# Optimization experiments

Measured on AMD Instinct MI355X. Metric: run time of the kernel, lower is better.

The kernel has to match this reference:

```python
import jax, jax.numpy as jnp
import numpy as np

H = 16  # number of heads (init kwarg h)

def vdp_matmul(a, va, b, vb):
    # VDP propagation through a matmul of two independent Gaussian tensors:
    # mean = a @ b ; var = va @ vb + va @ b^2 + a^2 @ vb
    mu = jnp.matmul(a, b)
    var = jnp.matmul(va, vb) + jnp.matmul(va, b * b) + jnp.matmul(a * a, vb)
    return mu, var

def softmax_vdp(a, va):
    # diagonal-Jacobian VDP softmax: p = softmax(a); var = (p(1-p))^2 * va
    p = jax.nn.softmax(a, axis=-1)
    return p, (p * (1.0 - p)) ** 2 * va

def setup_inputs() -> dict:
    key = jax.random.key(0)
    ks = jax.random.split(key, 8)
    B, S, D = 2, 1024, 1024
    sc = 1.0 / np.sqrt(D)
    return {
        "x": jax.random.normal(ks[0], (B, S, D), jnp.float32),
        "var_x": jax.random.uniform(ks[1], (B, S, D), jnp.float32) * 0.1,
        "wq_mu": jax.random.normal(ks[2], (D, D), jnp.float32) * sc,
        "wq_var": jax.random.uniform(ks[3], (D, D), jnp.float32) * 0.01,
        "wk_mu": jax.random.normal(ks[4], (D, D), jnp.float32) * sc,
        "wk_var": jax.random.uniform(ks[5], (D, D), jnp.float32) * 0.01,
        "wv_mu": jax.random.normal(ks[6], (D, D), jnp.float32) * sc,
        "wv_var": jax.random.uniform(ks[7], (D, D), jnp.float32) * 0.01,
    }

def _split_heads(t, h):
    B, S, D = t.shape
    return t.reshape(B, S, h, D // h).transpose(0, 2, 1, 3)  # [B,h,S,dh]

def reference(x, var_x, wq_mu, wq_var, wk_mu, wk_var, wv_mu, wv_var):
    D = x.shape[-1]
    rd = jnp.sqrt(jnp.asarray(D, x.dtype))
    # LinearVDP (bias=False): treat weight^T as the second VDP matmul operand
    q, vq = vdp_matmul(x, var_x, wq_mu.T, wq_var.T)
    k, vk = vdp_matmul(x, var_x, wk_mu.T, wk_var.T)
    v, vv = vdp_matmul(x, var_x, wv_mu.T, wv_var.T)
    q, vq = _split_heads(q, H), _split_heads(vq, H)
    k, vk = _split_heads(k, H), _split_heads(vk, H)
    v, vv = _split_heads(v, H), _split_heads(vv, H)
    # scores: q @ k^T with VDP variance, scaled (masking=False path)
    a, va = vdp_matmul(q, vq, k.transpose(0, 1, 3, 2), vk.transpose(0, 1, 3, 2))
    a, va = a / rd, va / (rd * rd)
    a, va = softmax_vdp(a, va)
    # attention-weighted values with VDP variance
    a, va = vdp_matmul(a, va, v, vv)
    a = a.transpose(0, 2, 1, 3).reshape(x.shape)      # [B,S,D]
    va = va.transpose(0, 2, 1, 3).reshape(x.shape)    # [B,S,D]
    return x + a, va
```

## Files before the change

kernel.cpp:

```cpp
#include <hip/hip_runtime.h>
#include <stdint.h>

typedef unsigned short u16;
typedef __attribute__((ext_vector_type(4))) float f32x4;
typedef __attribute__((ext_vector_type(8))) short s16x8;
typedef __attribute__((ext_vector_type(2))) unsigned u32x2;

#define MFMA16(a,b,c) __builtin_amdgcn_mfma_f32_16x16x32_bf16(a,b,c,0,0,0)

__device__ inline u16 f2b(float f){
  unsigned u = __float_as_uint(f);
  unsigned r = u + 0x7fffu + ((u>>16)&1u);
  return (u16)(r>>16);
}
__device__ inline float b2f(u16 b){
  return __uint_as_float(((unsigned)b)<<16);
}
__device__ inline unsigned cvtpk(float lo, float hi){
  unsigned r;
  asm("v_cvt_pk_bf16_f32 %0, %1, %2" : "=v"(r) : "v"(lo), "v"(hi));
  return r;
}
__device__ inline void load_lds16(const void* g, void* l){
  __builtin_amdgcn_global_load_lds((const __attribute__((address_space(1))) void*)g,
                                   (__attribute__((address_space(3))) void*)l, 16, 0, 0);
}

__global__ void prep_in_kernel(const float* __restrict__ x, const float* __restrict__ vx,
                               const float* __restrict__ w0mu, const float* __restrict__ w0va,
                               const float* __restrict__ w1mu, const float* __restrict__ w1va,
                               const float* __restrict__ w2mu, const float* __restrict__ w2va,
                               u16* __restrict__ xb, u16* __restrict__ acat,
                               u16* __restrict__ wmub, u16* __restrict__ bcat){
  int bid = blockIdx.x;
  if (bid < 2048){
    int i4 = bid*256 + threadIdx.x;
    int base = i4*4;
    int j = base & 1023;
    float4 xv = *(const float4*)(x + base);
    float4 vv = *(const float4*)(vx + base);
    u32x2 xpk = {cvtpk(xv.x,xv.y), cvtpk(xv.z,xv.w)};
    *(u32x2*)(xb + base) = xpk;
    size_t ar = (size_t)(base >> 10)*2048;
    *(u32x2*)(acat + ar + j) = (u32x2){cvtpk(vv.x,vv.y), cvtpk(vv.z,vv.w)};
    *(u32x2*)(acat + ar + 1024 + j) =
        (u32x2){cvtpk(xv.x*xv.x, xv.y*xv.y), cvtpk(xv.z*xv.z, xv.w*xv.w)};
  } else {
    int t = bid - 2048;
    int z = t >> 10;
    int i4 = (t & 1023)*256 + threadIdx.x;
    int base = i4*4;
    const float* wmu = z==0?w0mu:(z==1?w1mu:w2mu);
    const float* wva = z==0?w0va:(z==1?w1va:w2va);
    u16* wb = wmub + (size_t)z*1048576;
    u16* bc = bcat + (size_t)z*2097152;
    int j = base & 1023;
    float4 mu = *(const float4*)(wmu + base);
    float4 va = *(const float4*)(wva + base);
    *(u32x2*)(wb + base) = (u32x2){cvtpk(mu.x,mu.y), cvtpk(mu.z,mu.w)};
    size_t br = (size_t)(base >> 10)*2048;
    *(u32x2*)(bc + br + j) =
        (u32x2){cvtpk(va.x+mu.x*mu.x, va.y+mu.y*mu.y),
                cvtpk(va.z+mu.z*mu.z, va.w+mu.w*mu.w)};
    *(u32x2*)(bc + br + 1024 + j) = (u32x2){cvtpk(va.x,va.y), cvtpk(va.z,va.w)};
  }
}

__global__ __launch_bounds__(256) void gemm_nt6_kernel(
    const u16* __restrict__ xb, const u16* __restrict__ acat,
    const u16* __restrict__ wmub, const u16* __restrict__ bcat,
    u16* __restrict__ cbase){
  int bid = blockIdx.x;
  int z = bid % 6;
  int xy = bid / 6;
  int bx = xy & 15, by = xy >> 4;
  const u16* A = z<3 ? xb : acat;
  int K = z<3 ? 1024 : 2048;
  const u16* B = z<3 ? wmub + (size_t)z*1048576 : bcat + (size_t)(z-3)*2097152;
  u16* C = cbase + (size_t)z*2097152;
  const int N = 1024;
  __shared__ __align__(16) u16 As0[128*32], As1[128*32], As2[128*32];
  __shared__ __align__(16) u16 Bs0[128*32], Bs1[128*32], Bs2[128*32];
  int tid = threadIdx.x;
  int wid = tid>>6, lane = tid&63;
  int wr = wid>>1, wc = wid&1;
  int fr = lane&15, kg = lane>>4;
  int m0 = bx*128, n0 = by*128;
  int srow = lane>>2;
  int scol = (lane&3)*8;

  auto stage = [&](u16* Ad, u16* Bd, int k0){
    #pragma unroll
    for (int c=0;c<2;c++){
      int r = c*64 + wid*16 + srow;
      load_lds16(A + (size_t)(m0+r)*K + k0 + scol, (char*)Ad + (size_t)(c*64+wid*16)*64);
      load_lds16(B + (size_t)(n0+r)*K + k0 + scol, (char*)Bd + (size_t)(c*64+wid*16)*64);
    }
  };

  int nt = K >> 5;
  u16 *Ar=As0, *An=As1, *At=As2, *Br=Bs0, *Bn=Bs1, *Bt=Bs2;
  stage(Ar, Br, 0);
  stage(An, Bn, 32);
  f32x4 acc[4][4] = {};
  for (int t=0; t<nt; t++){
    if (t < nt-1) asm volatile("s_waitcnt vmcnt(4)" ::: "memory");
    else          asm volatile("s_waitcnt vmcnt(0)" ::: "memory");
    __builtin_amdgcn_s_barrier();
    if (t+2 < nt) stage(At, Bt, (t+2)*32);
    s16x8 af[4], bfv[4];
    #pragma unroll
    for (int i=0;i<4;i++){
      af[i]  = *(const s16x8*)(Ar + (wr*64 + i*16 + fr)*32 + kg*8);
      bfv[i] = *(const s16x8*)(Br + (wc*64 + i*16 + fr)*32 + kg*8);
    }
    #pragma unroll
    for (int i=0;i<4;i++)
      #pragma unroll
      for (int j=0;j<4;j++)
        acc[i][j] = MFMA16(bfv[j], af[i], acc[i][j]);
    u16* ta = Ar; Ar = An; An = At; At = ta;
    u16* tb = Br; Br = Bn; Bn = Bt; Bt = tb;
  }
  #pragma unroll
  for (int i=0;i<4;i++){
    int mrow = m0 + wr*64 + i*16 + fr;
    #pragma unroll
    for (int j=0;j<4;j++){
      int ncol = n0 + wc*64 + j*16 + kg*4;
      u32x2 pk = {cvtpk(acc[i][j][0],acc[i][j][1]), cvtpk(acc[i][j][2],acc[i][j][3])};
      *(u32x2*)(C + (size_t)mrow*N + ncol) = pk;
    }
  }
}

__global__ void mid_kernel(const u16* __restrict__ kb, const u16* __restrict__ vkb,
                           u16* __restrict__ kw2,
                           const u16* __restrict__ vb, const u16* __restrict__ vvb,
                           u16* __restrict__ vT, u16* __restrict__ vw2T,
                           u16* __restrict__ vvT){
  __shared__ u16 t[32][33];
  int bid = blockIdx.x;
  if (bid < 6144){
    int z = bid / 2048, wI = bid % 2048;
    int bx = wI & 31, by = wI >> 5;
    u16* out = z==0?vT:(z==1?vw2T:vvT);
    int tx = threadIdx.x & 31, ty = threadIdx.x >> 5;
    int c0 = bx*32, r0 = by*32;
    #pragma unroll
    for (int rr=0; rr<32; rr+=8){
      size_t idx = (size_t)(r0+ty+rr)*1024 + c0+tx;
      u16 val;
      if (z==0)      val = vb[idx];
      else if (z==2) val = vvb[idx];
      else {
        float v  = b2f(vb[idx]);
        float vv = b2f(vvb[idx]);
        val = f2b(vv + v*v);
      }
      t[ty+rr][tx] = val;
    }
    __syncthreads();
    #pragma unroll
    for (int rr=0; rr<32; rr+=8)
      out[(size_t)(c0+ty+rr)*2048 + r0+tx] = t[tx][ty+rr];
  } else {
    int i = (bid - 6144)*256 + threadIdx.x;
    float kk = b2f(kb[i]);
    float vk = b2f(vkb[i]);
    kw2[i] = f2b(vk + kk*kk);
  }
}

__global__ __launch_bounds__(256) void attn_vdp_kernel(
  const u16* __restrict__ qb, const u16* __restrict__ vqb,
  const u16* __restrict__ kb, const u16* __restrict__ kw2, const u16* __restrict__ vkb,
  const u16* __restrict__ vT, const u16* __restrict__ vw2T, const u16* __restrict__ vvT,
  const float* __restrict__ x, float* __restrict__ out0, float* __restrict__ out1){
  int qblk = blockIdx.x, h = blockIdx.y, b = blockIdx.z;
  int wid = threadIdx.x>>6, lane = threadIdx.x&63;
  int fr = lane&15, kg = lane>>4;
  int qrow0 = qblk*64 + wid*16;
  size_t mbase = (size_t)b*1024;

  __shared__ __align__(16) u16 bufA[3][4096];
  __shared__ __align__(16) u16 bufB[3][4096];
  __shared__ __align__(16) u16 plds[4][3][16][72];

  const int srow = lane>>3;
  const int sci  = (lane&7) ^ srow;
  const int c0   = wid*2;

  auto stA1 = [&](int jt, u16* dst){
    size_t base = (mbase + (size_t)jt*64)*1024 + h*64;
    #pragma unroll
    for (int c2=0;c2<2;c2++){
      int c = c0+c2;
      size_t go = base + (size_t)(c*8+srow)*1024 + sci*8;
      load_lds16(kb + go, (char*)dst + c*1024);
    }
  };
  auto stK3 = [&](int jt){
    size_t base = (mbase + (size_t)jt*64)*1024 + h*64;
    #pragma unroll
    for (int c2=0;c2<2;c2++){
      int c = c0+c2;
      size_t go = base + (size_t)(c*8+srow)*1024 + sci*8;
      load_lds16(kb  + go, (char*)bufA[0] + c*1024);
      load_lds16(kw2 + go, (char*)bufA[1] + c*1024);
      load_lds16(vkb + go, (char*)bufA[2] + c*1024);
    }
  };
  auto stV3 = [&](int jt){
    size_t base = (size_t)(h*64)*2048 + mbase + (size_t)jt*64;
    #pragma unroll
    for (int c2=0;c2<2;c2++){
      int c = c0+c2;
      size_t go = base + (size_t)(c*8+srow)*2048 + sci*8;
      load_lds16(vT   + go, (char*)bufB[0] + c*1024);
      load_lds16(vw2T + go, (char*)bufB[1] + c*1024);
      load_lds16(vvT  + go, (char*)bufB[2] + c*1024);
    }
  };
  auto frag = [&](const u16* t, int ni, int kf)->s16x8{
    int R = ni*16+fr;
    return *(const s16x8*)(t + R*64 + (((kg + kf*4) ^ (R&7))<<3));
  };

  s16x8 qa[2], vqa[2], qsa[2];
  {
    size_t ro = (mbase + qrow0 + fr)*1024 + h*64 + kg*8;
    #pragma unroll
    for (int kf=0;kf<2;kf++){
      qa[kf]  = *(const s16x8*)(qb  + ro + kf*32);
      vqa[kf] = *(const s16x8*)(vqb + ro + kf*32);
      #pragma unroll
      for (int e=0;e<8;e+=2){
        float lo = b2f((u16)qa[kf][e]);
        float hi = b2f((u16)qa[kf][e+1]);
        unsigned pk = cvtpk(lo*lo, hi*hi);
        qsa[kf][e]   = (short)(pk & 0xffffu);
        qsa[kf][e+1] = (short)(pk >> 16);
      }
    }
  }
  const float scale = 0.03125f;

  float lsum = 0.f;
  stA1(0, bufA[0]);
  __syncthreads();
  for (int jt=0;jt<16;jt++){
    const u16* cur = (jt&1) ? bufB[0] : bufA[0];
    if (jt<15) stA1(jt+1, (jt&1) ? bufA[0] : bufB[0]);
    else       stK3(0);
    f32x4 sacc[4] = {};
    __builtin_amdgcn_s_setprio(1);
    #pragma unroll
    for (int ni=0;ni<4;ni++)
      #pragma unroll
      for (int kf=0;kf<2;kf++)
        sacc[ni] = MFMA16(frag(cur,ni,kf), qa[kf], sacc[ni]);
    __builtin_amdgcn_s_setprio(0);
    #pragma unroll
    for (int ni=0;ni<4;ni++)
      #pragma unroll
      for (int r=0;r<4;r++)
        lsum += __expf(sacc[ni][r]*scale);
    __syncthreads();
  }
  lsum += __shfl_xor(lsum, 16);
  lsum += __shfl_xor(lsum, 32);
  const float linv = 1.f/lsum;

  f32x4 omu[4] = {}, ova[4] = {};
  for (int jt=0;jt<16;jt++){
    stV3(jt);
    f32x4 sacc[4] = {}, vacc[4] = {};
    __builtin_amdgcn_s_setprio(1);
    #pragma unroll
    for (int ni=0;ni<4;ni++)
      #pragma unroll
      for (int kf=0;kf<2;kf++){
        sacc[ni] = MFMA16(frag(bufA[0],ni,kf), qa[kf],  sacc[ni]);
        vacc[ni] = MFMA16(frag(bufA[1],ni,kf), vqa[kf], vacc[ni]);
        vacc[ni] = MFMA16(frag(bufA[2],ni,kf), qsa[kf], vacc[ni]);
      }
    __builtin_amdgcn_s_setprio(0);
    #pragma unroll
    for (int ni=0;ni<4;ni++){
      float pv[4], vpv[4], psv[4];
      #pragma unroll
      for (int r=0;r<4;r++){
        float p  = __expf(sacc[ni][r]*scale) * linv;
        float va = vacc[ni][r] * 9.765625e-4f;
        float g  = p*(1.f-p);
        pv[r]  = p;
        vpv[r] = g*g*va;
        psv[r] = p*p;
      }
      *(u32x2*)&plds[wid][0][fr][ni*16+kg*4] = (u32x2){cvtpk(pv[0],pv[1]),   cvtpk(pv[2],pv[3])};
      *(u32x2*)&plds[wid][1][fr][ni*16+kg*4] = (u32x2){cvtpk(vpv[0],vpv[1]), cvtpk(vpv[2],vpv[3])};
      *(u32x2*)&plds[wid][2][fr][ni*16+kg*4] = (u32x2){cvtpk(psv[0],psv[1]), cvtpk(psv[2],psv[3])};
    }
    s16x8 pa[2], vpa[2], pqa[2];
    #pragma unroll
    for (int kf=0;kf<2;kf++){
      pa[kf]  = *(const s16x8*)&plds[wid][0][fr][kf*32 + kg*8];
      vpa[kf] = *(const s16x8*)&plds[wid][1][fr][kf*32 + kg*8];
      pqa[kf] = *(const s16x8*)&plds[wid][2][fr][kf*32 + kg*8];
    }
    __syncthreads();
    if (jt<15) stK3(jt+1);
    __builtin_amdgcn_s_setprio(1);
    #pragma unroll
    for (int ni=0;ni<4;ni++)
      #pragma unroll
      for (int kf=0;kf<2;kf++){
        omu[ni] = MFMA16(pa[kf],  frag(bufB[0],ni,kf), omu[ni]);
        ova[ni] = MFMA16(vpa[kf], frag(bufB[1],ni,kf), ova[ni]);
        ova[ni] = MFMA16(pqa[kf], frag(bufB[2],ni,kf), ova[ni]);
      }
    __builtin_amdgcn_s_setprio(0);
    __syncthreads();
  }

  #pragma unroll
  for (int ni=0;ni<4;ni++){
    #pragma unroll
    for (int r=0;r<4;r++){
      size_t idx = (mbase + qrow0 + kg*4 + r)*1024 + h*64 + ni*16 + fr;
      out0[idx] = x[idx] + omu[ni][r];
      out1[idx] = ova[ni][r];
    }
  }
}

extern "C" void kernel_launch(void* const* d_in, const int* in_sizes, int n_in,
                              void* d_out, int out_size, void* d_ws, size_t ws_size,
                              hipStream_t stream){
  const float* x    = (const float*)d_in[0];
  const float* vx   = (const float*)d_in[1];
  const float* wqmu = (const float*)d_in[2];
  const float* wqva = (const float*)d_in[3];
  const float* wkmu = (const float*)d_in[4];
  const float* wkva = (const float*)d_in[5];
  const float* wvmu = (const float*)d_in[6];
  const float* wvva = (const float*)d_in[7];
  float* out0 = (float*)d_out;
  float* out1 = out0 + 2u*1024u*1024u;

  char* w = (char*)d_ws;
  const size_t MB = 1024*1024;
  u16* xb   = (u16*)(w +  0*MB);
  u16* acat = (u16*)(w +  4*MB);
  u16* wmub = (u16*)(w + 12*MB);
  u16* bcat = (u16*)(w + 18*MB);
  u16* qb_  = (u16*)(w + 30*MB);
  u16* kb_  = (u16*)(w + 34*MB);
  u16* vb_  = (u16*)(w + 38*MB);
  u16* vqb  = (u16*)(w + 42*MB);
  u16* vkb  = (u16*)(w + 46*MB);
  u16* vvb  = (u16*)(w + 50*MB);
  u16* kw2  = (u16*)(w + 54*MB);
  u16* vT   = (u16*)(w + 58*MB);
  u16* vw2T = (u16*)(w + 62*MB);
  u16* vvT  = (u16*)(w + 66*MB);

  prep_in_kernel<<<5120, 256, 0, stream>>>(x, vx, wqmu, wqva, wkmu, wkva, wvmu, wvva,
                                           xb, acat, wmub, bcat);
  gemm_nt6_kernel<<<768, 256, 0, stream>>>(xb, acat, wmub, bcat, qb_);
  mid_kernel<<<14336, 256, 0, stream>>>(kb_, vkb, kw2, vb_, vvb, vT, vw2T, vvT);
  attn_vdp_kernel<<<dim3(16,16,2), 256, 0, stream>>>(qb_, vqb, kb_, kw2, vkb,
                                                     vT, vw2T, vvT, x, out0, out1);
}
```

Before: 213.8 us.

## Swizzle LDS tiles and switch projection GEMM to double buffering

Adds an XOR-style column swizzle for the global-to-LDS loads and the matching fragment reads in the fused projection GEMM, to reduce LDS bank conflicts. It also replaces the three-stage ring buffer, which used explicit vmcnt waits, with a two-buffer scheme synchronised by __syncthreads each iteration. The swizzle targets conflict stalls, but the shallower pipeline and full barrier, which also drains outstanding loads, may expose more global memory latency.

New measurement: 213.0 us. About the same (-0.3%).

```diff
diff --git a/kernel.cpp b/kernel.cpp
--- a/kernel.cpp
+++ b/kernel.cpp
@@ -79,48 +79,45 @@
   const u16* B = z<3 ? wmub + (size_t)z*1048576 : bcat + (size_t)(z-3)*2097152;
   u16* C = cbase + (size_t)z*2097152;
   const int N = 1024;
-  __shared__ __align__(16) u16 As0[128*32], As1[128*32], As2[128*32];
-  __shared__ __align__(16) u16 Bs0[128*32], Bs1[128*32], Bs2[128*32];
+  __shared__ __align__(16) u16 As[2][128*32];
+  __shared__ __align__(16) u16 Bs[2][128*32];
   int tid = threadIdx.x;
   int wid = tid>>6, lane = tid&63;
   int wr = wid>>1, wc = wid&1;
   int fr = lane&15, kg = lane>>4;
   int m0 = bx*128, n0 = by*128;
   int srow = lane>>2;
-  int scol = (lane&3)*8;
-
-  auto stage = [&](u16* Ad, u16* Bd, int k0){
+  int scol = (((lane&3) - ((lane>>3)&3)) & 3) * 8;
+  int ks  = ((kg + ((fr>>1)&3)) & 3) * 8;
+
+  auto stage = [&](int buf, int k0){
     #pragma unroll
     for (int c=0;c<2;c++){
       int r = c*64 + wid*16 + srow;
-      load_lds16(A + (size_t)(m0+r)*K + k0 + scol, (char*)Ad + (size_t)(c*64+wid*16)*64);
-      load_lds16(B + (size_t)(n0+r)*K + k0 + scol, (char*)Bd + (size_t)(c*64+wid*16)*64);
-    }
-  };
-
-  int nt = K >> 5;
-  u16 *Ar=As0, *An=As1, *At=As2, *Br=Bs0, *Bn=Bs1, *Bt=Bs2;
-  stage(Ar, Br, 0);
-  stage(An, Bn, 32);
+      load_lds16(A + (size_t)(m0+r)*K + k0 + scol, (char*)As[buf] + (size_t)(c*64+wid*16)*64);
+      load_lds16(B + (size_t)(n0+r)*K + k0 + scol, (char*)Bs[buf] + (size_t)(c*64+wid*16)*64);
+    }
+  };
+
   f32x4 acc[4][4] = {};
-  for (int t=0; t<nt; t++){
-    if (t < nt-1) asm volatile("s_waitcnt vmcnt(4)" ::: "memory");
-    else          asm volatile("s_waitcnt vmcnt(0)" ::: "memory");
-    __builtin_amdgcn_s_barrier();
-    if (t+2 < nt) stage(At, Bt, (t+2)*32);
+  stage(0, 0);
+  __syncthreads();
+  int cur = 0;
+  for (int k0=0; k0<K; k0+=32){
+    if (k0+32<K) stage(cur^1, k0+32);
     s16x8 af[4], bfv[4];
     #pragma unroll
     for (int i=0;i<4;i++){
-      af[i]  = *(const s16x8*)(Ar + (wr*64 + i*16 + fr)*32 + kg*8);
-      bfv[i] = *(const s16x8*)(Br + (wc*64 + i*16 + fr)*32 + kg*8);
+      af[i]  = *(const s16x8*)(As[cur] + (wr*64 + i*16 + fr)*32 + ks);
+      bfv[i] = *(const s16x8*)(Bs[cur] + (wc*64 + i*16 + fr)*32 + ks);
     }
     #pragma unroll
     for (int i=0;i<4;i++)
       #pragma unroll
       for (int j=0;j<4;j++)
         acc[i][j] = MFMA16(bfv[j], af[i], acc[i][j]);
-    u16* ta = Ar; Ar = An; An = At; At = ta;
-    u16* tb = Br; Br = Bn; Bn = Bt; Bt = tb;
+    __syncthreads();
+    cur ^= 1;
   }
   #pragma unroll
   for (int i=0;i<4;i++){
```
